# Kernel optimization log

Measured on AMD Instinct MI355X. Metric: run time of the kernel, lower is better.

The kernel has to match this reference:

```python
import jax, jax.numpy as jnp
import numpy as np

NUM_CLASSES = 80
STRIDES = (8, 16, 32)
INPUT_SIZE = 640
DIST_THRESH_SQ = 64.0 * 64.0  # assignment uses euclidean dist < 64; compare squared


def make_anchors(input_size):
    pts = []
    for s in STRIDES:
        n = input_size // s
        yv, xv = np.meshgrid(np.arange(n), np.arange(n), indexing='ij')
        g = np.stack([xv, yv], -1).reshape(-1, 2).astype(np.float32) * s + s // 2
        pts.append(g)
    return jnp.asarray(np.concatenate(pts, 0))  # [A, 2]


def bce_logits(x, t):
    # BCEWithLogits, elementwise: -(t*log_sigmoid(x) + (1-t)*log_sigmoid(-x))
    return -(t * jax.nn.log_sigmoid(x) + (1.0 - t) * jax.nn.log_sigmoid(-x))


def iou_loss(pred_boxes, target_boxes):
    # pred: (cx, cy, log_w, log_h); target: (cx, cy, w, h) in pixels
    pc = pred_boxes[:, :2]
    ps = jnp.exp(pred_boxes[:, 2:4])
    p1 = pc - ps / 2.0
    p2 = pc + ps / 2.0
    t1 = target_boxes[:, :2] - target_boxes[:, 2:4] / 2.0
    t2 = target_boxes[:, :2] + target_boxes[:, 2:4] / 2.0
    i1 = jnp.maximum(p1, t1)
    i2 = jnp.minimum(p2, t2)
    inter = jnp.clip(i2[:, 0] - i1[:, 0], 0.0) * jnp.clip(i2[:, 1] - i1[:, 1], 0.0)
    pa = (p2[:, 0] - p1[:, 0]) * (p2[:, 1] - p1[:, 1])
    ta = (t2[:, 0] - t1[:, 0]) * (t2[:, 1] - t1[:, 1])
    union = pa + ta - inter
    return 1.0 - inter / (union + 1e-06)


def setup_inputs() -> dict:
    key = jax.random.key(0)
    k1, k2, k3, k4, k5 = jax.random.split(key, 5)
    B, M = 64, 50
    A = sum((INPUT_SIZE // s) ** 2 for s in STRIDES)  # 8400
    predictions = jax.random.normal(k1, (B, A, 5 + NUM_CLASSES), dtype=jnp.float32)
    cls = jax.random.randint(k2, (B, M), 0, NUM_CLASSES).astype(jnp.float32)
    valid = jax.random.uniform(k3, (B, M)) < 0.6
    cls = jnp.where(valid, cls, -1.0)
    centers = jax.random.uniform(k4, (B, M, 2), minval=0.05, maxval=0.95)
    wh = jax.random.uniform(k5, (B, M, 2), minval=0.02, maxval=0.3)
    targets = jnp.concatenate([cls[..., None], centers, wh], axis=-1).astype(jnp.float32)
    return {"predictions": predictions, "targets": targets, "input_size": 640}


def _per_image(pred, tgt, anchors, num_classes, input_size):
    # pred: [A, 5+C], tgt: [M, 5]
    valid = tgt[:, 0] >= 0.0                              # [M]
    gt_cls = tgt[:, 0].astype(jnp.int32)                  # [M]
    gt_boxes = tgt[:, 1:5] * input_size                   # [M, 4] pixels
    diff = gt_boxes[:, None, :2] - anchors[None, :, :]    # [M, A, 2]
    d2 = jnp.sum(diff * diff, axis=-1)                    # [M, A] squared dist
    d2 = jnp.where(valid[:, None], d2, jnp.inf)
    matched = jnp.argmin(d2, axis=0)                      # [A]
    min_d2 = jnp.min(d2, axis=0)                          # [A]
    pos = min_d2 < DIST_THRESH_SQ                         # [A]
    posf = pos.astype(pred.dtype)
    num_pos = posf.sum()

    obj_loss = bce_logits(pred[:, 4], posf).mean()

    cls_t = jax.nn.one_hot(gt_cls[matched], num_classes, dtype=pred.dtype)  # [A, C]
    cls_bce = bce_logits(pred[:, 5:], cls_t)                                # [A, C]
    denom = jnp.maximum(num_pos, 1.0)
    cls_loss = jnp.where(num_pos > 0,
                         (cls_bce * posf[:, None]).sum() / (denom * num_classes), 0.0)

    iou_l = iou_loss(pred[:, :4], gt_boxes[matched])      # [A]
    box_loss = jnp.where(num_pos > 0, (iou_l * posf).sum() / denom, 0.0)
    return obj_loss, cls_loss, box_loss, num_pos


def reference(predictions, targets, input_size):
    anchors = make_anchors(int(input_size))               # [A, 2]
    fsize = jnp.float32(input_size)
    obj, cls, box, npos = jax.vmap(
        lambda p, t: _per_image(p, t, anchors, NUM_CLASSES, fsize)
    )(predictions, targets)
    obj_loss = obj.sum()
    cls_loss = cls.sum()
    box_loss = box.sum()
    num_fg = npos.sum()
    total = 5.0 * box_loss + obj_loss + cls_loss
    return total, box_loss, obj_loss, cls_loss, num_fg
```

## Files before the change

### kernel.cpp

```cpp
#include <hip/hip_runtime.h>
#include <math.h>

#define NUM_CLASSES 80
#define MT 50
#define ATOT 8400
#define CH 85
#define EPI (ATOT * CH)
#define EPG (EPI / 4)
#define BLOCK 256
#define CHUNK 256
#define NBY 33
#define NX 88
#define G 8

__device__ __forceinline__ float softplus_fast(float x) {
    return fmaxf(x, 0.0f) + __logf(1.0f + __expf(-fabsf(x)));
}

__global__ __launch_bounds__(BLOCK) void yolox_match(
        const float* __restrict__ pred,
        const float* __restrict__ tgt,
        const int*   __restrict__ isz,
        int*   __restrict__ gmask,
        float* __restrict__ accM) {
    const int b  = blockIdx.y;
    const int by = blockIdx.x;
    const int a0 = by * CHUNK;
    const int nanch = min(CHUNK, ATOT - a0);

    __shared__ float2 sxy[64];
    __shared__ float2 swh[64];
    __shared__ float  scls[64];
    __shared__ int    snv;

    if (threadIdx.x < 64) {
        const int m = threadIdx.x;
        const float fsize = (float)(*isz);
        float c = -1.0f, x = 0.f, y = 0.f, w = 0.f, h = 0.f;
        if (m < MT) {
            const float* tb = tgt + (size_t)b * MT * 5 + (size_t)m * 5;
            c = tb[0];
            x = tb[1] * fsize; y = tb[2] * fsize;
            w = tb[3] * fsize; h = tb[4] * fsize;
        }
        const bool valid = (m < MT) && (c >= 0.0f);
        const unsigned long long ballot = __ballot(valid);
        const int slot = __popcll(ballot & ((1ull << threadIdx.x) - 1ull));
        if (valid) {
            sxy[slot]  = make_float2(x, y);
            swh[slot]  = make_float2(w, h);
            scls[slot] = c;
        }
        if (m == 0) snv = (int)__popcll(ballot);
    }
    __syncthreads();
    const int nv = snv;

    float box_s = 0.f, np_s = 0.f;

    const int a = a0 + threadIdx.x;
    if (threadIdx.x < nanch) {
        float ax, ay;
        if (a < 6400)      { const int yy = a / 80;              const int xx = a - yy * 80;  ax = (float)(xx * 8  + 4);  ay = (float)(yy * 8  + 4); }
        else if (a < 8000) { const int i2 = a - 6400; const int yy = i2 / 40; const int xx = i2 - yy * 40; ax = (float)(xx * 16 + 8);  ay = (float)(yy * 16 + 8); }
        else               { const int i2 = a - 8000; const int yy = i2 / 20; const int xx = i2 - yy * 20; ax = (float)(xx * 32 + 16); ay = (float)(yy * 32 + 16); }

        float best = INFINITY;
        int bestm = 0;
        for (int m = 0; m < nv; ++m) {
            const float2 g = sxy[m];
            const float dx = g.x - ax, dy = g.y - ay;
            const float d2 = dx * dx + dy * dy;
            if (d2 < best) { best = d2; bestm = m; }
        }
        const bool pos = best < 4096.0f;

        gmask[(size_t)b * ATOT + a] = pos ? (int)scls[bestm] : -1;

        if (pos) {
            np_s = 1.0f;
            const float* p = pred + ((size_t)b * ATOT + (size_t)a) * CH;
            const float pcx = p[0], pcy = p[1];
            const float pw = __expf(p[2]), ph = __expf(p[3]);
            const float2 g  = sxy[bestm];
            const float2 wh = swh[bestm];
            const float p1x = pcx - pw * 0.5f, p2x = pcx + pw * 0.5f;
            const float p1y = pcy - ph * 0.5f, p2y = pcy + ph * 0.5f;
            const float t1x = g.x - wh.x * 0.5f, t2x = g.x + wh.x * 0.5f;
            const float t1y = g.y - wh.y * 0.5f, t2y = g.y + wh.y * 0.5f;
            const float iw = fminf(p2x, t2x) - fmaxf(p1x, t1x);
            const float ih = fminf(p2y, t2y) - fmaxf(p1y, t1y);
            const float inter = fmaxf(iw, 0.f) * fmaxf(ih, 0.f);
            const float pa = (p2x - p1x) * (p2y - p1y);
            const float ta = (t2x - t1x) * (t2y - t1y);
            const float uni = pa + ta - inter;
            box_s = 1.0f - inter / (uni + 1e-6f);
        }
    }

    float v2 = box_s, v3 = np_s;
    for (int off = 32; off > 0; off >>= 1) {
        v2 += __shfl_down(v2, off, 64);
        v3 += __shfl_down(v3, off, 64);
    }
    __shared__ float sred[BLOCK / 64][2];
    const int wave = threadIdx.x >> 6;
    const int lane = threadIdx.x & 63;
    if (lane == 0) { sred[wave][0] = v2; sred[wave][1] = v3; }
    __syncthreads();
    if (threadIdx.x == 0) {
        float t2 = 0.f, t3 = 0.f;
        #pragma unroll
        for (int w = 0; w < BLOCK / 64; ++w) { t2 += sred[w][0]; t3 += sred[w][1]; }
        float* slot = accM + ((size_t)b * NBY + by) * 2;
        slot[0] = t2; slot[1] = t3;
    }
}

__global__ __launch_bounds__(BLOCK) void yolox_bulk(
        const float* __restrict__ pred,
        const int*   __restrict__ gmask,
        float* __restrict__ accB) {
    const int b   = blockIdx.y;
    const int tid = threadIdx.x;
    const int base_g = blockIdx.x * (BLOCK * G);

    const float* pbase = pred + (size_t)b * EPI;
    const int*   mbase = gmask + (size_t)b * ATOT;

    int  mk[G], c0k[G], lek[G];
    bool need[G];

    #pragma unroll
    for (int k = 0; k < G; ++k) {
        const int g  = base_g + k * BLOCK + tid;
        const bool ok = g < EPG;
        const int le = g << 2;
        const unsigned la = __umulhi((unsigned)le, 3233857729u) >> 6;
        lek[k] = le;
        c0k[k] = le - (int)la * CH;
        mk[k]  = ok ? mbase[la] : -1;
        need[k] = ok && ((c0k[k] >= 1 && c0k[k] <= 4) || (mk[k] >= 0 && c0k[k] >= 2));
    }

    float4 x[G];
    #pragma unroll
    for (int k = 0; k < G; ++k) {
        x[k] = need[k] ? *(const float4*)(pbase + lek[k])
                       : make_float4(0.f, 0.f, 0.f, 0.f);
    }

    float obj_s = 0.f, cls_s = 0.f;
    #pragma unroll
    for (int k = 0; k < G; ++k) {
        if (!need[k]) continue;
        const int c0 = c0k[k];
        const int m  = mk[k];
        const bool mpos = m >= 0;
        const float xs[4] = {x[k].x, x[k].y, x[k].z, x[k].w};
        #pragma unroll
        for (int j = 0; j < 4; ++j) {
            const int c = c0 + j;
            const float xv = xs[j];
            if (c == 4) {
                obj_s += softplus_fast(xv) - (mpos ? xv : 0.0f);
            } else if (c >= 5 && c < CH && mpos) {
                cls_s += softplus_fast(xv) - ((c - 5 == m) ? xv : 0.0f);
            }
        }
    }

    float v0 = obj_s, v1 = cls_s;
    for (int off = 32; off > 0; off >>= 1) {
        v0 += __shfl_down(v0, off, 64);
        v1 += __shfl_down(v1, off, 64);
    }
    __shared__ float sred[BLOCK / 64][2];
    const int wave = threadIdx.x >> 6;
    const int lane = threadIdx.x & 63;
    if (lane == 0) { sred[wave][0] = v0; sred[wave][1] = v1; }
    __syncthreads();
    if (threadIdx.x == 0) {
        float t0 = 0.f, t1 = 0.f;
        #pragma unroll
        for (int w = 0; w < BLOCK / 64; ++w) { t0 += sred[w][0]; t1 += sred[w][1]; }
        float* slot = accB + ((size_t)b * NX + blockIdx.x) * 2;
        slot[0] = t0; slot[1] = t1;
    }
}

__global__ __launch_bounds__(BLOCK) void yolox_stage2(
        const float* __restrict__ accM,
        const float* __restrict__ accB,
        float* __restrict__ out, int B) {
    float obj = 0.f, cls = 0.f, box = 0.f, np = 0.f;
    for (int bb = threadIdx.x; bb < B; bb += BLOCK) {
        float bs = 0.f, ps = 0.f;
        const float* sM = accM + (size_t)bb * NBY * 2;
        #pragma unroll
        for (int j = 0; j < NBY; ++j) { bs += sM[j * 2 + 0]; ps += sM[j * 2 + 1]; }
        float os = 0.f, cs = 0.f;
        const float* sB = accB + (size_t)bb * NX * 2;
        #pragma unroll 8
        for (int j = 0; j < NX; ++j) { os += sB[j * 2 + 0]; cs += sB[j * 2 + 1]; }
        obj += os * (1.0f / (float)ATOT);
        const float denom = fmaxf(ps, 1.0f);
        cls += (ps > 0.f) ? cs / (denom * (float)NUM_CLASSES) : 0.f;
        box += (ps > 0.f) ? bs / denom : 0.f;
        np  += ps;
    }
    float v0 = obj, v1 = cls, v2 = box, v3 = np;
    for (int off = 32; off > 0; off >>= 1) {
        v0 += __shfl_down(v0, off, 64);
        v1 += __shfl_down(v1, off, 64);
        v2 += __shfl_down(v2, off, 64);
        v3 += __shfl_down(v3, off, 64);
    }
    __shared__ float sred[BLOCK / 64][4];
    const int wave = threadIdx.x >> 6;
    const int lane = threadIdx.x & 63;
    if (lane == 0) {
        sred[wave][0] = v0; sred[wave][1] = v1;
        sred[wave][2] = v2; sred[wave][3] = v3;
    }
    __syncthreads();
    if (threadIdx.x == 0) {
        float t0 = 0.f, t1 = 0.f, t2 = 0.f, t3 = 0.f;
        #pragma unroll
        for (int w = 0; w < BLOCK / 64; ++w) {
            t0 += sred[w][0]; t1 += sred[w][1];
            t2 += sred[w][2]; t3 += sred[w][3];
        }
        out[0] = 5.0f * t2 + t0 + t1;
        out[1] = t2;
        out[2] = t0;
        out[3] = t1;
        out[4] = t3;
    }
}

extern "C" void kernel_launch(void* const* d_in, const int* in_sizes, int n_in,
                              void* d_out, int out_size, void* d_ws, size_t ws_size,
                              hipStream_t stream) {
    const float* pred = (const float*)d_in[0];
    const float* tgt  = (const float*)d_in[1];
    const int*   isz  = (const int*)d_in[2];
    float* out = (float*)d_out;

    const int B = in_sizes[1] / (MT * 5);

    int*   gmask = (int*)d_ws;
    float* accM  = (float*)((char*)d_ws + (size_t)B * ATOT * sizeof(int));
    float* accB  = accM + (size_t)B * NBY * 2;

    dim3 gridM(NBY, B);
    yolox_match<<<gridM, BLOCK, 0, stream>>>(pred, tgt, isz, gmask, accM);

    dim3 gridB(NX, B);
    yolox_bulk<<<gridB, BLOCK, 0, stream>>>(pred, gmask, accB);

    yolox_stage2<<<1, BLOCK, 0, stream>>>(accM, accB, out, B);
}
```

Measured before the change: 270.3 us.

## Fuse anchor matching and BCE bulk pass into one kernel using shared mask

Merges the matching kernel and the bulk objectness/class BCE kernel into a single kernel where each block matches its 256-anchor chunk, keeps the matched class mask in shared memory, and then streams that chunk's prediction rows. This removes the global gmask write and reread, one kernel launch, and the separate partial-sum buffers, and stage2 now reduces one combined accumulator. The tradeoff is fewer blocks (33 per image instead of 88) with more serial work per block, which may reduce memory-level parallelism. Chunk offsets stay 16-byte aligned because 256*85 is divisible by 4.

```diff
diff --git a/kernel.cpp b/kernel.cpp
--- a/kernel.cpp
+++ b/kernel.cpp
@@ -6,23 +6,19 @@
 #define ATOT 8400
 #define CH 85
 #define EPI (ATOT * CH)
-#define EPG (EPI / 4)
 #define BLOCK 256
 #define CHUNK 256
 #define NBY 33
-#define NX 88
-#define G 8
 
 __device__ __forceinline__ float softplus_fast(float x) {
     return fmaxf(x, 0.0f) + __logf(1.0f + __expf(-fabsf(x)));
 }
 
-__global__ __launch_bounds__(BLOCK) void yolox_match(
+__global__ __launch_bounds__(BLOCK) void yolox_fused(
         const float* __restrict__ pred,
         const float* __restrict__ tgt,
         const int*   __restrict__ isz,
-        int*   __restrict__ gmask,
-        float* __restrict__ accM) {
+        float* __restrict__ acc) {
     const int b  = blockIdx.y;
     const int by = blockIdx.x;
     const int a0 = by * CHUNK;
@@ -32,6 +28,7 @@
     __shared__ float2 swh[64];
     __shared__ float  scls[64];
     __shared__ int    snv;
+    __shared__ int    smask[CHUNK];
 
     if (threadIdx.x < 64) {
         const int m = threadIdx.x;
@@ -57,6 +54,7 @@
     const int nv = snv;
 
     float box_s = 0.f, np_s = 0.f;
+    int myMask = -1;
 
     const int a = a0 + threadIdx.x;
     if (threadIdx.x < nanch) {
@@ -74,8 +72,7 @@
             if (d2 < best) { best = d2; bestm = m; }
         }
         const bool pos = best < 4096.0f;
-
-        gmask[(size_t)b * ATOT + a] = pos ? (int)scls[bestm] : -1;
+        myMask = pos ? (int)scls[bestm] : -1;
 
         if (pos) {
             np_s = 1.0f;
@@ -97,67 +94,62 @@
             box_s = 1.0f - inter / (uni + 1e-6f);
         }
     }
-
-    float v2 = box_s, v3 = np_s;
-    for (int off = 32; off > 0; off >>= 1) {
-        v2 += __shfl_down(v2, off, 64);
-        v3 += __shfl_down(v3, off, 64);
-    }
-    __shared__ float sred[BLOCK / 64][2];
-    const int wave = threadIdx.x >> 6;
-    const int lane = threadIdx.x & 63;
-    if (lane == 0) { sred[wave][0] = v2; sred[wave][1] = v3; }
-    __syncthreads();
-    if (threadIdx.x == 0) {
-        float t2 = 0.f, t3 = 0.f;
-        #pragma unroll
-        for (int w = 0; w < BLOCK / 64; ++w) { t2 += sred[w][0]; t3 += sred[w][1]; }
-        float* slot = accM + ((size_t)b * NBY + by) * 2;
-        slot[0] = t2; slot[1] = t3;
-    }
-}
-
-__global__ __launch_bounds__(BLOCK) void yolox_bulk(
-        const float* __restrict__ pred,
-        const int*   __restrict__ gmask,
-        float* __restrict__ accB) {
-    const int b   = blockIdx.y;
-    const int tid = threadIdx.x;
-    const int base_g = blockIdx.x * (BLOCK * G);
-
-    const float* pbase = pred + (size_t)b * EPI;
-    const int*   mbase = gmask + (size_t)b * ATOT;
-
-    int  mk[G], c0k[G], lek[G];
-    bool need[G];
-
-    #pragma unroll
-    for (int k = 0; k < G; ++k) {
-        const int g  = base_g + k * BLOCK + tid;
-        const bool ok = g < EPG;
-        const int le = g << 2;
-        const unsigned la = __umulhi((unsigned)le, 3233857729u) >> 6;
-        lek[k] = le;
-        c0k[k] = le - (int)la * CH;
-        mk[k]  = ok ? mbase[la] : -1;
-        need[k] = ok && ((c0k[k] >= 1 && c0k[k] <= 4) || (mk[k] >= 0 && c0k[k] >= 2));
-    }
-
-    float4 x[G];
-    #pragma unroll
-    for (int k = 0; k < G; ++k) {
-        x[k] = need[k] ? *(const float4*)(pbase + lek[k])
-                       : make_float4(0.f, 0.f, 0.f, 0.f);
-    }
+    smask[threadIdx.x] = myMask;
+    __syncthreads();
+
+    const float* pblock = pred + (size_t)b * EPI + (size_t)a0 * CH;
+    const int NG = (nanch * CH) >> 2;
 
     float obj_s = 0.f, cls_s = 0.f;
-    #pragma unroll
-    for (int k = 0; k < G; ++k) {
-        if (!need[k]) continue;
-        const int c0 = c0k[k];
-        const int m  = mk[k];
+
+    int gi = threadIdx.x;
+    for (; gi + 3 * BLOCK < NG; gi += 4 * BLOCK) {
+        int   ok[4], c0k[4], mk[4];
+        bool  need[4];
+        #pragma unroll
+        for (int k = 0; k < 4; ++k) {
+            const int o = (gi + k * BLOCK) << 2;
+            const unsigned la = __umulhi((unsigned)o, 3233857729u) >> 6;
+            ok[k]  = o;
+            c0k[k] = o - (int)la * CH;
+            mk[k]  = smask[la];
+            need[k] = (c0k[k] >= 1 && c0k[k] <= 4) || (mk[k] >= 0 && c0k[k] >= 2);
+        }
+        float4 x[4];
+        #pragma unroll
+        for (int k = 0; k < 4; ++k) {
+            x[k] = need[k] ? *(const float4*)(pblock + ok[k])
+                           : make_float4(0.f, 0.f, 0.f, 0.f);
+        }
+        #pragma unroll
+        for (int k = 0; k < 4; ++k) {
+            if (!need[k]) continue;
+            const int c0 = c0k[k];
+            const int m  = mk[k];
+            const bool mpos = m >= 0;
+            const float xs[4] = {x[k].x, x[k].y, x[k].z, x[k].w};
+            #pragma unroll
+            for (int j = 0; j < 4; ++j) {
+                const int c = c0 + j;
+                const float xv = xs[j];
+                if (c == 4) {
+                    obj_s += softplus_fast(xv) - (mpos ? xv : 0.0f);
+                } else if (c >= 5 && c < CH && mpos) {
+                    cls_s += softplus_fast(xv) - ((c - 5 == m) ? xv : 0.0f);
+                }
+            }
+        }
+    }
+    for (; gi < NG; gi += BLOCK) {
+        const int o = gi << 2;
+        const unsigned la = __umulhi((unsigned)o, 3233857729u) >> 6;
+        const int c0 = o - (int)la * CH;
+        const int m  = smask[la];
+        const bool need1 = (c0 >= 1 && c0 <= 4) || (m >= 0 && c0 >= 2);
+        if (!need1) continue;
+        const float4 x = *(const float4*)(pblock + o);
         const bool mpos = m >= 0;
-        const float xs[4] = {x[k].x, x[k].y, x[k].z, x[k].w};
+        const float xs[4] = {x.x, x.y, x.z, x.w};
         #pragma unroll
         for (int j = 0; j < 4; ++j) {
             const int c = c0 + j;
@@ -170,39 +162,45 @@
         }
     }
 
-    float v0 = obj_s, v1 = cls_s;
+    float v0 = box_s, v1 = np_s, v2 = obj_s, v3 = cls_s;
     for (int off = 32; off > 0; off >>= 1) {
         v0 += __shfl_down(v0, off, 64);
         v1 += __shfl_down(v1, off, 64);
-    }
-    __shared__ float sred[BLOCK / 64][2];
+        v2 += __shfl_down(v2, off, 64);
+        v3 += __shfl_down(v3, off, 64);
+    }
+    __shared__ float sred[BLOCK / 64][4];
     const int wave = threadIdx.x >> 6;
     const int lane = threadIdx.x & 63;
-    if (lane == 0) { sred[wave][0] = v0; sred[wave][1] = v1; }
+    if (lane == 0) {
+        sred[wave][0] = v0; sred[wave][1] = v1;
+        sred[wave][2] = v2; sred[wave][3] = v3;
+    }
     __syncthreads();
     if (threadIdx.x == 0) {
-        float t0 = 0.f, t1 = 0.f;
-        #pragma unroll
-        for (int w = 0; w < BLOCK / 64; ++w) { t0 += sred[w][0]; t1 += sred[w][1]; }
-        float* slot = accB + ((size_t)b * NX + blockIdx.x) * 2;
-        slot[0] = t0; slot[1] = t1;
+        float t0 = 0.f, t1 = 0.f, t2 = 0.f, t3 = 0.f;
+        #pragma unroll
+        for (int w = 0; w < BLOCK / 64; ++w) {
+            t0 += sred[w][0]; t1 += sred[w][1];
+            t2 += sred[w][2]; t3 += sred[w][3];
+        }
+        float* slot = acc + ((size_t)b * NBY + by) * 4;
+        slot[0] = t0; slot[1] = t1; slot[2] = t2; slot[3] = t3;
     }
 }
 
 __global__ __launch_bounds__(BLOCK) void yolox_stage2(
-        const float* __restrict__ accM,
-        const float* __restrict__ accB,
+        const float* __restrict__ acc,
         float* __restrict__ out, int B) {
     float obj = 0.f, cls = 0.f, box = 0.f, np = 0.f;
     for (int bb = threadIdx.x; bb < B; bb += BLOCK) {
-        float bs = 0.f, ps = 0.f;
-        const float* sM = accM + (size_t)bb * NBY * 2;
-        #pragma unroll
-        for (int j = 0; j < NBY; ++j) { bs += sM[j * 2 + 0]; ps += sM[j * 2 + 1]; }
-        float os = 0.f, cs = 0.f;
-        const float* sB = accB + (size_t)bb * NX * 2;
-        #pragma unroll 8
-        for (int j = 0; j < NX; ++j) { os += sB[j * 2 + 0]; cs += sB[j * 2 + 1]; }
+        float bs = 0.f, ps = 0.f, os = 0.f, cs = 0.f;
+        const float* s = acc + (size_t)bb * NBY * 4;
+        #pragma unroll
+        for (int j = 0; j < NBY; ++j) {
+            bs += s[j * 4 + 0]; ps += s[j * 4 + 1];
+            os += s[j * 4 + 2]; cs += s[j * 4 + 3];
+        }
         obj += os * (1.0f / (float)ATOT);
         const float denom = fmaxf(ps, 1.0f);
         cls += (ps > 0.f) ? cs / (denom * (float)NUM_CLASSES) : 0.f;
@@ -249,15 +247,10 @@
 
     const int B = in_sizes[1] / (MT * 5);
 
-    int*   gmask = (int*)d_ws;
-    float* accM  = (float*)((char*)d_ws + (size_t)B * ATOT * sizeof(int));
-    float* accB  = accM + (size_t)B * NBY * 2;
-
-    dim3 gridM(NBY, B);
-    yolox_match<<<gridM, BLOCK, 0, stream>>>(pred, tgt, isz, gmask, accM);
-
-    dim3 gridB(NX, B);
-    yolox_bulk<<<gridB, BLOCK, 0, stream>>>(pred, gmask, accB);
-
-    yolox_stage2<<<1, BLOCK, 0, stream>>>(accM, accB, out, B);
-}
+    float* acc = (float*)d_ws;
+
+    dim3 grid(NBY, B);
+    yolox_fused<<<grid, BLOCK, 0, stream>>>(pred, tgt, isz, acc);
+
+    yolox_stage2<<<1, BLOCK, 0, stream>>>(acc, out, B);
+}
```

After: 268.7 us. About the same (-0.6%).
